# Performance work log

Hardware: AMD Instinct MI355X
Metric: run time of the kernel (lower is better)

The kernel has to match this reference:

```python
import jax, jax.numpy as jnp
import numpy as np

N_NODES = 50000
N_EDGES = 800000
D_IN = 128
H1 = H2 = H3 = 128
N_CLASS = 16
N_GRAPHS = 500


def setup_inputs() -> dict:
    key = jax.random.key(0)
    ks = jax.random.split(key, 10)
    x = jax.random.normal(ks[0], (N_NODES, D_IN), dtype=jnp.float32)
    edge_src = jax.random.randint(ks[1], (N_EDGES,), 0, N_NODES)
    edge_dst = jax.random.randint(ks[2], (N_EDGES,), 0, N_NODES)
    idx = jnp.sort(jax.random.randint(ks[3], (N_NODES,), 0, N_GRAPHS))
    s = 0.02  # small init scale
    W1 = jax.random.normal(ks[4], (D_IN, H1), dtype=jnp.float32) * s
    W2 = jax.random.normal(ks[5], (H1, H2), dtype=jnp.float32) * s
    W3 = jax.random.normal(ks[6], (H2, H3), dtype=jnp.float32) * s
    W4 = jax.random.normal(ks[7], (H3, N_CLASS), dtype=jnp.float32) * s
    b1 = jnp.zeros((H1,), jnp.float32)
    b2 = jnp.zeros((H2,), jnp.float32)
    b3 = jnp.zeros((H3,), jnp.float32)
    b4 = jnp.zeros((N_CLASS,), jnp.float32)
    return {"x": x, "edge_src": edge_src, "edge_dst": edge_dst, "idx": idx,
            "W1": W1, "b1": b1, "W2": W2, "b2": b2,
            "W3": W3, "b3": b3, "W4": W4, "b4": b4}


def reference(x, edge_src, edge_dst, idx, W1, b1, W2, b2, W3, b3, W4, b4):
    # adj_tilde @ h  with binary adjacency + identity, in edge-list form:
    # row i accumulates h[j] for every edge (i<-j), plus h[i] from the eye.
    def propagate(h):
        return h + jax.ops.segment_sum(h[edge_src], edge_dst, num_segments=h.shape[0])

    z1 = jax.nn.relu(propagate(x) @ W1 + b1)            # [N, H1]
    h = propagate(z1) @ W2 + b2                          # [N, H2]
    # scatter_add pooling per graph id (fixed number of graphs for jit)
    pooled = jax.ops.segment_sum(h, idx, num_segments=N_GRAPHS)  # [G, H2]
    zg = jax.nn.relu(pooled @ W3 + b3)                   # [G, H3]
    out = zg @ W4 + b4                                   # [G, C]
    return jax.nn.log_softmax(out, axis=1)
```

## Files before the change

### kernel.cpp

```cpp
#include <hip/hip_runtime.h>
#include <hip/hip_bf16.h>
#include <math.h>

#define NN 50000
#define NE 800000
#define DD 128
#define NG 500
#define NC 16

#define BBITS 6
#define BDSTS 64
#define NBK ((NN + BDSTS - 1) / BDSTS)
#define NCHUNK 256
#define EPB (NE / NCHUNK)
#define ECAP 1536
#define GEMMBLK ((NN + 127) / 128)

using short8 = __attribute__((ext_vector_type(8))) short;
using f32x4  = __attribute__((ext_vector_type(4))) float;

static __device__ __forceinline__ ushort f2bf(float f) {
    __hip_bfloat16 h = __float2bfloat16(f);
    ushort r;
    __builtin_memcpy(&r, &h, sizeof(r));
    return r;
}
static __device__ __forceinline__ float bflo(uint v) { return __uint_as_float(v << 16); }
static __device__ __forceinline__ float bfhi(uint v) { return __uint_as_float(v & 0xffff0000u); }
static __device__ __forceinline__ uint packbf(float lo, float hi) {
    return ((uint)f2bf(hi) << 16) | (uint)f2bf(lo);
}

static __device__ __forceinline__ void add8(float* acc, uint4 v) {
    acc[0] += bflo(v.x); acc[1] += bfhi(v.x);
    acc[2] += bflo(v.y); acc[3] += bfhi(v.y);
    acc[4] += bflo(v.z); acc[5] += bfhi(v.z);
    acc[6] += bflo(v.w); acc[7] += bfhi(v.w);
}

static __device__ __forceinline__ int lower_bound_idx(const int* __restrict__ idx, int g) {
    if (g >= NG) return NN;
    int lo = 0, hi = NN;
    while (lo < hi) {
        int mid = (lo + hi) >> 1;
        if (idx[mid] < g) lo = mid + 1; else hi = mid;
    }
    return lo;
}

static __device__ __forceinline__ int chunk_of_block(int blk) {
    return (blk & 7) * 32 + (blk >> 3);
}

__global__ __launch_bounds__(256) void k0_prep_kernel(const int* __restrict__ edst,
                                                      int* __restrict__ cnt,
                                                      const float* __restrict__ W1,
                                                      ushort* __restrict__ W1t,
                                                      const int* __restrict__ idx,
                                                      int* __restrict__ gstart) {
    int t = threadIdx.x;
    if (blockIdx.x < NCHUNK) {
        __shared__ int hist[NBK];
        int chunk = chunk_of_block(blockIdx.x);
        const int e0 = chunk * EPB;
        for (int b = t; b < NBK; b += 256) hist[b] = 0;
        __syncthreads();
        for (int i = t; i < EPB; i += 256) atomicAdd(&hist[edst[e0 + i] >> BBITS], 1);
        __syncthreads();
        for (int b = t; b < NBK; b += 256) cnt[(size_t)chunk * NBK + b] = hist[b];
    } else if (blockIdx.x < NCHUNK + 64) {
        int flat = (blockIdx.x - NCHUNK) * 256 + t;
        if (flat < 128 * 128) {
            int k = flat >> 7, n = flat & 127;
            W1t[n * 128 + k] = f2bf(W1[flat]);
        }
    } else {
        int g = (blockIdx.x - NCHUNK - 64) * 256 + t;
        if (g <= NG) gstart[g] = lower_bound_idx(idx, g);
    }
}

static __device__ __forceinline__ void gemm_body(int blk, int tid,
                                                 const float* __restrict__ X,
                                                 const ushort* __restrict__ W1t,
                                                 ushort* __restrict__ Y, int M) {
    const int wave = tid >> 6, lane = tid & 63;
    const int wm = wave >> 1, wn = wave & 1;
    const int m0 = blk * 128 + wm * 64;
    const int n0 = wn * 64;
    const int lr = lane & 15;
    const int lk = (lane >> 4) * 8;

    int rows[4];
    bool valid[4];
    #pragma unroll
    for (int m = 0; m < 4; ++m) {
        rows[m] = m0 + m * 16 + lr;
        valid[m] = rows[m] < M;
    }

    f32x4 acc[4][4] = {};

    #pragma unroll
    for (int kc = 0; kc < 4; ++kc) {
        const int kb = kc * 32 + lk;
        short8 a[4];
        #pragma unroll
        for (int m = 0; m < 4; ++m) {
            union { short8 v; ushort u[8]; } ua;
            if (valid[m]) {
                const float* p = &X[(size_t)rows[m] * 128 + kb];
                float4 v0 = *reinterpret_cast<const float4*>(p);
                float4 v1 = *reinterpret_cast<const float4*>(p + 4);
                ua.u[0] = f2bf(v0.x); ua.u[1] = f2bf(v0.y);
                ua.u[2] = f2bf(v0.z); ua.u[3] = f2bf(v0.w);
                ua.u[4] = f2bf(v1.x); ua.u[5] = f2bf(v1.y);
                ua.u[6] = f2bf(v1.z); ua.u[7] = f2bf(v1.w);
            } else {
                #pragma unroll
                for (int j = 0; j < 8; ++j) ua.u[j] = 0;
            }
            a[m] = ua.v;
        }
        short8 b[4];
        #pragma unroll
        for (int n = 0; n < 4; ++n) {
            b[n] = *reinterpret_cast<const short8*>(&W1t[(size_t)(n0 + n * 16 + lr) * 128 + kb]);
        }
        #pragma unroll
        for (int m = 0; m < 4; ++m)
            #pragma unroll
            for (int n = 0; n < 4; ++n)
                acc[m][n] = __builtin_amdgcn_mfma_f32_16x16x32_bf16(a[m], b[n], acc[m][n], 0, 0, 0);
    }

    const int rbase = (lane >> 4) * 4;
    #pragma unroll
    for (int m = 0; m < 4; ++m) {
        #pragma unroll
        for (int r = 0; r < 4; ++r) {
            int row = m0 + m * 16 + rbase + r;
            if (row < M) {
                #pragma unroll
                for (int n = 0; n < 4; ++n) {
                    Y[(size_t)row * 128 + n0 + n * 16 + lr] = f2bf(acc[m][n][r]);
                }
            }
        }
    }
}

__global__ __launch_bounds__(256) void k1_gemm_scan1_kernel(const float* __restrict__ X,
                                                            const ushort* __restrict__ W1t,
                                                            ushort* __restrict__ Y,
                                                            const int* __restrict__ cnt,
                                                            int* __restrict__ bpos,
                                                            int* __restrict__ btot) {
    if (blockIdx.x < GEMMBLK) {
        gemm_body(blockIdx.x, threadIdx.x, X, W1t, Y, NN);
    } else {
        __shared__ int s[256];
        int b = blockIdx.x - GEMMBLK, t = threadIdx.x;
        int v = cnt[(size_t)t * NBK + b];
        s[t] = v;
        __syncthreads();
        for (int d = 1; d < 256; d <<= 1) {
            int x = (t >= d) ? s[t - d] : 0;
            __syncthreads();
            s[t] += x;
            __syncthreads();
        }
        bpos[b * NCHUNK + t] = s[t] - v;
        if (t == 255) btot[b] = s[255];
    }
}

__global__ __launch_bounds__(256) void csr_scatter_kernel(const int* __restrict__ esrc,
                                                          const int* __restrict__ edst,
                                                          const int* __restrict__ btot,
                                                          const int* __restrict__ bpos,
                                                          int* __restrict__ bbase,
                                                          uint* __restrict__ baux) {
    __shared__ int lbase[NBK];
    __shared__ int cur[NBK];
    __shared__ int tsA[256], tsB[256];
    int t = threadIdx.x;
    int chunk = chunk_of_block(blockIdx.x);
    const int e0 = chunk * EPB;

    int loc[4];
    int sum = 0;
    #pragma unroll
    for (int j = 0; j < 4; ++j) {
        int b = t * 4 + j;
        loc[j] = (b < NBK) ? btot[b] : 0;
        sum += loc[j];
    }
    tsA[t] = sum;
    __syncthreads();
    int* sbuf = tsA;
    int* dbuf = tsB;
    for (int d = 1; d < 256; d <<= 1) {
        dbuf[t] = sbuf[t] + ((t >= d) ? sbuf[t - d] : 0);
        __syncthreads();
        int* tmp = sbuf; sbuf = dbuf; dbuf = tmp;
    }
    int excl = sbuf[t] - sum;
    #pragma unroll
    for (int j = 0; j < 4; ++j) {
        int b = t * 4 + j;
        if (b < NBK) {
            if (blockIdx.x == 0) bbase[b] = excl;
            lbase[b] = excl + bpos[b * NCHUNK + chunk];
            cur[b] = 0;
        }
        excl += loc[j];
    }
    __syncthreads();

    for (int i = t; i < EPB; i += 256) {
        int d = edst[e0 + i], s = esrc[e0 + i];
        int b = d >> BBITS;
        int r = atomicAdd(&cur[b], 1);
        baux[lbase[b] + r] = ((uint)(d & (BDSTS - 1)) << 16) | (uint)s;
    }
}

__global__ __launch_bounds__(256) void bucket_sort_kernel(const uint* __restrict__ baux,
                                                          const int* __restrict__ btot,
                                                          const int* __restrict__ bbase,
                                                          int* __restrict__ offsets,
                                                          ushort* __restrict__ csr) {
    __shared__ uint ent[ECAP];
    __shared__ int hist[BDSTS], lofs[BDSTS], cur[BDSTS];
    int b = blockIdx.x, t = threadIdx.x;
    int n = btot[b];
    int base = bbase[b];
    if (t < BDSTS) hist[t] = 0;
    __syncthreads();
    for (int i = t; i < n; i += 256) {
        uint e = baux[base + i];
        ent[i] = e;
        atomicAdd(&hist[e >> 16], 1);
    }
    __syncthreads();
    if (t < BDSTS) lofs[t] = hist[t];
    __syncthreads();
    for (int d = 1; d < BDSTS; d <<= 1) {
        int x = 0;
        if (t < BDSTS && t >= d) x = lofs[t - d];
        __syncthreads();
        if (t < BDSTS) lofs[t] += x;
        __syncthreads();
    }
    int d0 = b * BDSTS;
    if (t < BDSTS) {
        int excl = lofs[t] - hist[t];
        lofs[t] = excl;
        cur[t] = 0;
        if (d0 + t < NN) offsets[d0 + t] = base + excl;
    }
    if (b == NBK - 1 && t == 0) offsets[NN] = NE;
    __syncthreads();
    for (int i = t; i < n; i += 256) {
        uint e = ent[i];
        int j = e >> 16;
        int pos = base + lofs[j] + atomicAdd(&cur[j], 1);
        csr[pos] = (ushort)(e & 0xffffu);
    }
}

__global__ __launch_bounds__(256) void prop1_kernel(const ushort* __restrict__ In,
                                                    const int* __restrict__ offs,
                                                    const ushort* __restrict__ csr,
                                                    const float* __restrict__ bias,
                                                    ushort* __restrict__ Out, int n) {
    int node = (blockIdx.x * blockDim.x + threadIdx.x) >> 6;
    int lane = threadIdx.x & 63;
    if (node >= n) return;
    const int q = lane >> 4;
    const int p = lane & 15;
    const uint4* Ir = reinterpret_cast<const uint4*>(In);

    float acc[8] = {};
    if (q == 0) add8(acc, Ir[(size_t)node * 16 + p]);

    int e = offs[node] + q, e1 = offs[node + 1];
    for (; e + 12 < e1; e += 16) {
        int s0 = csr[e], s1 = csr[e + 4], s2 = csr[e + 8], s3 = csr[e + 12];
        uint4 v0 = Ir[(size_t)s0 * 16 + p];
        uint4 v1 = Ir[(size_t)s1 * 16 + p];
        uint4 v2 = Ir[(size_t)s2 * 16 + p];
        uint4 v3 = Ir[(size_t)s3 * 16 + p];
        add8(acc, v0); add8(acc, v1); add8(acc, v2); add8(acc, v3);
    }
    for (; e < e1; e += 4) add8(acc, Ir[(size_t)csr[e] * 16 + p]);

    #pragma unroll
    for (int j = 0; j < 8; ++j) {
        acc[j] += __shfl_xor(acc[j], 16);
        acc[j] += __shfl_xor(acc[j], 32);
    }

    if (q == 0) {
        float4 bA = *reinterpret_cast<const float4*>(&bias[p * 8]);
        float4 bB = *reinterpret_cast<const float4*>(&bias[p * 8 + 4]);
        uint4 o;
        o.x = packbf(fmaxf(acc[0] + bA.x, 0.f), fmaxf(acc[1] + bA.y, 0.f));
        o.y = packbf(fmaxf(acc[2] + bA.z, 0.f), fmaxf(acc[3] + bA.w, 0.f));
        o.z = packbf(fmaxf(acc[4] + bB.x, 0.f), fmaxf(acc[5] + bB.y, 0.f));
        o.w = packbf(fmaxf(acc[6] + bB.z, 0.f), fmaxf(acc[7] + bB.w, 0.f));
        reinterpret_cast<uint4*>(Out)[(size_t)node * 16 + p] = o;
    }
}

__global__ __launch_bounds__(1024) void prop2head_kernel(const ushort* __restrict__ Z1,
                                                         const int* __restrict__ offs,
                                                         const ushort* __restrict__ csr,
                                                         const int* __restrict__ gstart,
                                                         const float* __restrict__ W2, const float* __restrict__ b2,
                                                         const float* __restrict__ W3, const float* __restrict__ b3,
                                                         const float* __restrict__ W4, const float* __restrict__ b4,
                                                         float* __restrict__ out) {
    int g = blockIdx.x, t = threadIdx.x;
    int gs = gstart[g], ge = gstart[g + 1];
    int w = t >> 6, lane = t & 63;
    int q = lane >> 4, p = lane & 15;
    int stream = w * 4 + q;
    const uint4* Zr = reinterpret_cast<const uint4*>(Z1);

    float acc[8] = {};
    for (int i = gs + stream; i < ge; i += 64) add8(acc, Zr[(size_t)i * 16 + p]);
    int E0 = offs[gs], E1 = offs[ge];
    int e = E0 + stream;
    for (; e + 448 < E1; e += 512) {
        int s0 = csr[e],       s1 = csr[e + 64],  s2 = csr[e + 128], s3 = csr[e + 192];
        int s4 = csr[e + 256], s5 = csr[e + 320], s6 = csr[e + 384], s7 = csr[e + 448];
        uint4 v0 = Zr[(size_t)s0 * 16 + p];
        uint4 v1 = Zr[(size_t)s1 * 16 + p];
        uint4 v2 = Zr[(size_t)s2 * 16 + p];
        uint4 v3 = Zr[(size_t)s3 * 16 + p];
        uint4 v4 = Zr[(size_t)s4 * 16 + p];
        uint4 v5 = Zr[(size_t)s5 * 16 + p];
        uint4 v6 = Zr[(size_t)s6 * 16 + p];
        uint4 v7 = Zr[(size_t)s7 * 16 + p];
        add8(acc, v0); add8(acc, v1); add8(acc, v2); add8(acc, v3);
        add8(acc, v4); add8(acc, v5); add8(acc, v6); add8(acc, v7);
    }
    for (; e + 192 < E1; e += 256) {
        int s0 = csr[e], s1 = csr[e + 64], s2 = csr[e + 128], s3 = csr[e + 192];
        uint4 v0 = Zr[(size_t)s0 * 16 + p];
        uint4 v1 = Zr[(size_t)s1 * 16 + p];
        uint4 v2 = Zr[(size_t)s2 * 16 + p];
        uint4 v3 = Zr[(size_t)s3 * 16 + p];
        add8(acc, v0); add8(acc, v1); add8(acc, v2); add8(acc, v3);
    }
    for (; e < E1; e += 64) add8(acc, Zr[(size_t)csr[e] * 16 + p]);

    #pragma unroll
    for (int j = 0; j < 8; ++j) {
        acc[j] += __shfl_xor(acc[j], 16);
        acc[j] += __shfl_xor(acc[j], 32);
    }
    __shared__ float red[16][128];
    if (q == 0) {
        #pragma unroll
        for (int j = 0; j < 8; ++j) red[w][p * 8 + j] = acc[j];
    }
    __syncthreads();

    __shared__ float vs[128], hs[128], zs[128], os[16];
    if (t < 128) {
        float s = 0.f;
        #pragma unroll
        for (int k = 0; k < 16; ++k) s += red[k][t];
        vs[t] = s;
    }
    __syncthreads();
    if (t < 128) {
        float c = (float)(ge - gs);
        float a = c * b2[t];
        #pragma unroll 8
        for (int k = 0; k < 128; ++k) a = fmaf(vs[k], W2[k * 128 + t], a);
        hs[t] = a;
    }
    __syncthreads();
    if (t < 128) {
        float z = b3[t];
        #pragma unroll 8
        for (int k = 0; k < 128; ++k) z = fmaf(hs[k], W3[k * 128 + t], z);
        zs[t] = fmaxf(z, 0.f);
    }
    __syncthreads();
    if (t < 16) {
        float oo = b4[t];
        #pragma unroll 8
        for (int k = 0; k < 128; ++k) oo = fmaf(zs[k], W4[k * 16 + t], oo);
        os[t] = oo;
    }
    __syncthreads();
    if (t < 16) {
        float m = -INFINITY;
        #pragma unroll
        for (int k = 0; k < 16; ++k) m = fmaxf(m, os[k]);
        float ssum = 0.f;
        #pragma unroll
        for (int k = 0; k < 16; ++k) ssum += expf(os[k] - m);
        out[g * 16 + t] = os[t] - m - logf(ssum);
    }
}

extern "C" void kernel_launch(void* const* d_in, const int* in_sizes, int n_in,
                              void* d_out, int out_size, void* d_ws, size_t ws_size,
                              hipStream_t stream) {
    const float* x    = (const float*)d_in[0];
    const int*   esrc = (const int*)d_in[1];
    const int*   edst = (const int*)d_in[2];
    const int*   idx  = (const int*)d_in[3];
    const float* W1   = (const float*)d_in[4];
    const float* b1   = (const float*)d_in[5];
    const float* W2   = (const float*)d_in[6];
    const float* b2   = (const float*)d_in[7];
    const float* W3   = (const float*)d_in[8];
    const float* b3   = (const float*)d_in[9];
    const float* W4   = (const float*)d_in[10];
    const float* b4   = (const float*)d_in[11];
    float* out = (float*)d_out;

    char* w = (char*)d_ws;
    auto alloc = [&](size_t bytes) -> void* {
        void* p = (void*)w;
        w += (bytes + 255) & ~(size_t)255;
        return p;
    };
    int* cnt      = (int*)alloc((size_t)NCHUNK * NBK * 4);
    int* bpos     = (int*)alloc((size_t)NBK * NCHUNK * 4);
    int* btot     = (int*)alloc((size_t)NBK * 4);
    int* bbase    = (int*)alloc((size_t)NBK * 4);
    int* gstart   = (int*)alloc((size_t)(NG + 1) * 4);
    uint* baux    = (uint*)alloc((size_t)NE * 4);
    int* offsets  = (int*)alloc((size_t)(NN + 1) * 4);
    ushort* csr   = (ushort*)alloc((size_t)NE * 2);
    ushort* w1t   = (ushort*)alloc((size_t)DD * DD * 2);
    ushort* y     = (ushort*)alloc((size_t)NN * DD * 2);
    ushort* z1    = (ushort*)alloc((size_t)NN * DD * 2);

    k0_prep_kernel<<<NCHUNK + 64 + 2, 256, 0, stream>>>(edst, cnt, W1, w1t, idx, gstart);

    k1_gemm_scan1_kernel<<<GEMMBLK + NBK, 256, 0, stream>>>(x, w1t, y, cnt, bpos, btot);

    csr_scatter_kernel<<<NCHUNK, 256, 0, stream>>>(esrc, edst, btot, bpos, bbase, baux);
    bucket_sort_kernel<<<NBK, 256, 0, stream>>>(baux, btot, bbase, offsets, csr);

    prop1_kernel<<<NN / 4, 256, 0, stream>>>(y, offsets, csr, b1, z1, NN);

    prop2head_kernel<<<NG, 1024, 0, stream>>>(z1, offsets, csr, gstart,
                                              W2, b2, W3, b3, W4, b4, out);
}
```

Measured before the change: 110.1 us.

## Split layer-1 GEMM blocks across scatter and sort kernels to overlap work

```diff
diff --git a/kernel.cpp b/kernel.cpp
--- a/kernel.cpp
+++ b/kernel.cpp
@@ -15,6 +15,8 @@
 #define EPB (NE / NCHUNK)
 #define ECAP 1536
 #define GEMMBLK ((NN + 127) / 128)
+#define GEMM_A 196
+#define GEMM_B (GEMMBLK - GEMM_A)
 
 using short8 = __attribute__((ext_vector_type(8))) short;
 using f32x4  = __attribute__((ext_vector_type(4))) float;
@@ -78,6 +80,24 @@
         int g = (blockIdx.x - NCHUNK - 64) * 256 + t;
         if (g <= NG) gstart[g] = lower_bound_idx(idx, g);
     }
+}
+
+__global__ __launch_bounds__(256) void k1_scan1_kernel(const int* __restrict__ cnt,
+                                                       int* __restrict__ bpos,
+                                                       int* __restrict__ btot) {
+    __shared__ int s[256];
+    int b = blockIdx.x, t = threadIdx.x;
+    int v = cnt[(size_t)t * NBK + b];
+    s[t] = v;
+    __syncthreads();
+    for (int d = 1; d < 256; d <<= 1) {
+        int x = (t >= d) ? s[t - d] : 0;
+        __syncthreads();
+        s[t] += x;
+        __syncthreads();
+    }
+    bpos[b * NCHUNK + t] = s[t] - v;
+    if (t == 255) btot[b] = s[255];
 }
 
 static __device__ __forceinline__ void gemm_body(int blk, int tid,
@@ -150,41 +170,23 @@
     }
 }
 
-__global__ __launch_bounds__(256) void k1_gemm_scan1_kernel(const float* __restrict__ X,
-                                                            const ushort* __restrict__ W1t,
-                                                            ushort* __restrict__ Y,
-                                                            const int* __restrict__ cnt,
-                                                            int* __restrict__ bpos,
-                                                            int* __restrict__ btot) {
-    if (blockIdx.x < GEMMBLK) {
-        gemm_body(blockIdx.x, threadIdx.x, X, W1t, Y, NN);
-    } else {
-        __shared__ int s[256];
-        int b = blockIdx.x - GEMMBLK, t = threadIdx.x;
-        int v = cnt[(size_t)t * NBK + b];
-        s[t] = v;
-        __syncthreads();
-        for (int d = 1; d < 256; d <<= 1) {
-            int x = (t >= d) ? s[t - d] : 0;
-            __syncthreads();
-            s[t] += x;
-            __syncthreads();
-        }
-        bpos[b * NCHUNK + t] = s[t] - v;
-        if (t == 255) btot[b] = s[255];
-    }
-}
-
-__global__ __launch_bounds__(256) void csr_scatter_kernel(const int* __restrict__ esrc,
-                                                          const int* __restrict__ edst,
-                                                          const int* __restrict__ btot,
-                                                          const int* __restrict__ bpos,
-                                                          int* __restrict__ bbase,
-                                                          uint* __restrict__ baux) {
+__global__ __launch_bounds__(256) void k2_scatter_gemm_kernel(const int* __restrict__ esrc,
+                                                              const int* __restrict__ edst,
+                                                              const int* __restrict__ btot,
+                                                              const int* __restrict__ bpos,
+                                                              int* __restrict__ bbase,
+                                                              uint* __restrict__ baux,
+                                                              const float* __restrict__ X,
+                                                              const ushort* __restrict__ W1t,
+                                                              ushort* __restrict__ Y) {
+    int t = threadIdx.x;
+    if (blockIdx.x >= NCHUNK) {
+        gemm_body(blockIdx.x - NCHUNK, t, X, W1t, Y, NN);
+        return;
+    }
     __shared__ int lbase[NBK];
     __shared__ int cur[NBK];
     __shared__ int tsA[256], tsB[256];
-    int t = threadIdx.x;
     int chunk = chunk_of_block(blockIdx.x);
     const int e0 = chunk * EPB;
 
@@ -226,14 +228,22 @@
     }
 }
 
-__global__ __launch_bounds__(256) void bucket_sort_kernel(const uint* __restrict__ baux,
-                                                          const int* __restrict__ btot,
-                                                          const int* __restrict__ bbase,
-                                                          int* __restrict__ offsets,
-                                                          ushort* __restrict__ csr) {
+__global__ __launch_bounds__(256) void k3_sort_gemm_kernel(const uint* __restrict__ baux,
+                                                           const int* __restrict__ btot,
+                                                           const int* __restrict__ bbase,
+                                                           int* __restrict__ offsets,
+                                                           ushort* __restrict__ csr,
+                                                           const float* __restrict__ X,
+                                                           const ushort* __restrict__ W1t,
+                                                           ushort* __restrict__ Y) {
+    int t = threadIdx.x;
+    if (blockIdx.x >= NBK) {
+        gemm_body(GEMM_A + (blockIdx.x - NBK), t, X, W1t, Y, NN);
+        return;
+    }
     __shared__ uint ent[ECAP];
     __shared__ int hist[BDSTS], lofs[BDSTS], cur[BDSTS];
-    int b = blockIdx.x, t = threadIdx.x;
+    int b = blockIdx.x;
     int n = btot[b];
     int base = bbase[b];
     if (t < BDSTS) hist[t] = 0;
@@ -447,10 +457,13 @@
 
     k0_prep_kernel<<<NCHUNK + 64 + 2, 256, 0, stream>>>(edst, cnt, W1, w1t, idx, gstart);
 
-    k1_gemm_scan1_kernel<<<GEMMBLK + NBK, 256, 0, stream>>>(x, w1t, y, cnt, bpos, btot);
-
-    csr_scatter_kernel<<<NCHUNK, 256, 0, stream>>>(esrc, edst, btot, bpos, bbase, baux);
-    bucket_sort_kernel<<<NBK, 256, 0, stream>>>(baux, btot, bbase, offsets, csr);
+    k1_scan1_kernel<<<NBK, 256, 0, stream>>>(cnt, bpos, btot);
+
+    k2_scatter_gemm_kernel<<<NCHUNK + GEMM_A, 256, 0, stream>>>(esrc, edst, btot, bpos,
+                                                                bbase, baux, x, w1t, y);
+
+    k3_sort_gemm_kernel<<<NBK + GEMM_B, 256, 0, stream>>>(baux, btot, bbase, offsets, csr,
+                                                          x, w1t, y);
 
     prop1_kernel<<<NN / 4, 256, 0, stream>>>(y, offsets, csr, b1, z1, NN);
 
```

New measurement: 119.5 us. 8.5% more time.
